# Kernel tuning notes

Measured on AMD Instinct MI355X. Metric: run time of the kernel, lower is better.

The kernel has to match this reference:

```python
import jax, jax.numpy as jnp
import numpy as np

B, S, D = 2, 2048, 2048
NH, NKV = 32, 8
HD = D // NH          # 64
NREP = NH // NKV      # 4


def _rope(x, cos, sin):
    # x: [B, S, H, HD]; cos/sin: [S, HD//2]
    x2 = x.reshape(*x.shape[:-1], HD // 2, 2)
    x0, x1 = x2[..., 0], x2[..., 1]
    c = cos[None, :, None, :]
    s = sin[None, :, None, :]
    r0 = x0 * c - x1 * s
    r1 = x0 * s + x1 * c
    return jnp.stack([r0, r1], axis=-1).reshape(x.shape)


def setup_inputs() -> dict:
    key = jax.random.key(0)
    ks = jax.random.split(key, 5)
    x = jax.random.normal(ks[0], (B, S, D), dtype=jnp.float32)
    wq = jax.random.normal(ks[1], (D, NH * HD), dtype=jnp.float32) * (D ** -0.5)
    wk = jax.random.normal(ks[2], (D, NKV * HD), dtype=jnp.float32) * (D ** -0.5)
    wv = jax.random.normal(ks[3], (D, NKV * HD), dtype=jnp.float32) * (D ** -0.5)
    wo = jax.random.normal(ks[4], (NH * HD, D), dtype=jnp.float32) * (D ** -0.5)
    # standard RoPE frequencies: theta = 10000^(-2i/HD)
    inv_freq = 1.0 / (10000.0 ** (np.arange(0, HD, 2, dtype=np.float32) / HD))
    angles = np.arange(S, dtype=np.float32)[:, None] * inv_freq[None, :]  # [S, HD/2]
    freqs_cos = jnp.asarray(np.cos(angles))
    freqs_sin = jnp.asarray(np.sin(angles))
    return {"x": x, "freqs_cos": freqs_cos, "freqs_sin": freqs_sin,
            "wq": wq, "wk": wk, "wv": wv, "wo": wo}


def reference(x, freqs_cos, freqs_sin, wq, wk, wv, wo):
    b, s, _ = x.shape
    xq = (x @ wq).reshape(b, s, NH, HD)
    xk = (x @ wk).reshape(b, s, NKV, HD)
    xv = (x @ wv).reshape(b, s, NKV, HD)
    xq = _rope(xq, freqs_cos, freqs_sin)
    xk = _rope(xk, freqs_cos, freqs_sin)
    # GQA repeat_kv: expand kv heads to NH
    keys = jnp.repeat(xk, NREP, axis=2)    # [B, S, NH, HD]
    values = jnp.repeat(xv, NREP, axis=2)
    scores = jnp.einsum('bqhd,bkhd->bhqk', xq, keys) / jnp.sqrt(jnp.float32(HD))
    causal = jnp.tril(jnp.ones((s, s), dtype=bool))
    scores = jnp.where(causal[None, None], scores, -jnp.inf)
    attn = jax.nn.softmax(scores.astype(jnp.float32), axis=-1).astype(xq.dtype)
    out = jnp.einsum('bhqk,bkhd->bqhd', attn, values).reshape(b, s, NH * HD)
    return out @ wo
```

## Files before the change

### kernel.cpp

```cpp
#include <hip/hip_runtime.h>
#include <hip/hip_bf16.h>

#define S_LEN 2048
#define DMODEL 2048
#define N_H 32
#define N_KV 8
#define H_D 64
#define ROWS 4096
#define QKV_LD 3072

typedef __bf16 bf16x8 __attribute__((ext_vector_type(8)));
typedef float f32x4 __attribute__((ext_vector_type(4)));

static __device__ __forceinline__ unsigned short f2bf(float f) {
  unsigned int u = __float_as_uint(f);
  u += 0x7FFFu + ((u >> 16) & 1u);
  return (unsigned short)(u >> 16);
}
static __device__ __forceinline__ float bf2f(unsigned short s) {
  return __uint_as_float((unsigned int)s << 16);
}

static __device__ __forceinline__ void async16(const void* g, void* l) {
  __builtin_amdgcn_global_load_lds(
      (const __attribute__((address_space(1))) unsigned int*)g,
      (__attribute__((address_space(3))) unsigned int*)l, 16, 0, 0);
}

#define VMB(N)                                                    \
  do {                                                            \
    asm volatile("s_waitcnt vmcnt(" #N ")" ::: "memory");         \
    __builtin_amdgcn_s_barrier();                                 \
    asm volatile("" ::: "memory");                                \
  } while (0)

__global__ __launch_bounds__(256) void cvt_bf16_k(
    const float* __restrict__ in, unsigned short* __restrict__ out) {
  const size_t i = ((size_t)blockIdx.x * 256 + threadIdx.x) * 8;
  const float4 a = *(const float4*)&in[i];
  const float4 b = *(const float4*)&in[i + 4];
  union { unsigned short u[8]; uint4 v; } p;
  p.u[0] = f2bf(a.x); p.u[1] = f2bf(a.y); p.u[2] = f2bf(a.z); p.u[3] = f2bf(a.w);
  p.u[4] = f2bf(b.x); p.u[5] = f2bf(b.y); p.u[6] = f2bf(b.z); p.u[7] = f2bf(b.w);
  *(uint4*)&out[i] = p.v;
}

__global__ __launch_bounds__(256) void prep_all_k(
    const float* __restrict__ x, const float* __restrict__ wq,
    const float* __restrict__ wk, const float* __restrict__ wv,
    const float* __restrict__ wo, unsigned short* __restrict__ xb,
    unsigned short* __restrict__ wqkvT, unsigned short* __restrict__ woT) {
  const int z = blockIdx.z;
  if (z == 4) {
    const size_t i =
        (((size_t)blockIdx.y * 64 + blockIdx.x) * 256 + threadIdx.x) * 8;
    const float4 a = *(const float4*)&x[i];
    const float4 b = *(const float4*)&x[i + 4];
    union { unsigned short u[8]; uint4 v; } p;
    p.u[0] = f2bf(a.x); p.u[1] = f2bf(a.y); p.u[2] = f2bf(a.z); p.u[3] = f2bf(a.w);
    p.u[4] = f2bf(b.x); p.u[5] = f2bf(b.y); p.u[6] = f2bf(b.z); p.u[7] = f2bf(b.w);
    *(uint4*)&xb[i] = p.v;
    return;
  }
  const float* in;
  unsigned short* out;
  int C;
  if (z == 0)      { in = wq; out = wqkvT;                  C = 2048; }
  else if (z == 1) { in = wk; out = wqkvT + 2048ull * 2048; C = 512;  }
  else if (z == 2) { in = wv; out = wqkvT + 2560ull * 2048; C = 512;  }
  else             { in = wo; out = woT;                    C = 2048; }
  if (blockIdx.x * 32 >= C) return;

  __shared__ unsigned short tile[32][33];
  const int tx = threadIdx.x & 31;
  const int ty = threadIdx.x >> 5;
  const int r0 = blockIdx.y * 32;
  const int c0 = blockIdx.x * 32;
#pragma unroll
  for (int i = 0; i < 32; i += 8)
    tile[ty + i][tx] = f2bf(in[(size_t)(r0 + ty + i) * C + c0 + tx]);
  __syncthreads();
#pragma unroll
  for (int i = 0; i < 32; i += 8)
    out[(size_t)(c0 + ty + i) * 2048 + r0 + tx] = tile[tx][ty + i];
}

#define SCALE_LOG2E 0.18033688011112042f

__global__ __launch_bounds__(256) void rope_vt_k(
    unsigned short* __restrict__ qkv, unsigned short* __restrict__ vT,
    const float* __restrict__ fc, const float* __restrict__ fs) {
  const int blk = blockIdx.x;
  if (blk < 20480) {
    const int PQ = ROWS * N_H * (H_D / 2);
    const int PK = ROWS * N_KV * (H_D / 2);
    const int idx = blk * 256 + threadIdx.x;
    if (idx >= PQ + PK) return;
    unsigned short* base;
    float c, sn;
    bool isq;
    if (idx < PQ) {
      const int i = idx & 31;
      const int h = (idx >> 5) & 31;
      const int row = idx >> 10;
      const int s = row & (S_LEN - 1);
      c = fc[s * 32 + i];
      sn = fs[s * 32 + i];
      base = qkv + (size_t)row * QKV_LD + h * H_D + 2 * i;
      isq = true;
    } else {
      const int p = idx - PQ;
      const int i = p & 31;
      const int h = (p >> 5) & 7;
      const int row = p >> 8;
      const int s = row & (S_LEN - 1);
      c = fc[s * 32 + i];
      sn = fs[s * 32 + i];
      base = qkv + (size_t)row * QKV_LD + 2048 + h * H_D + 2 * i;
      isq = false;
    }
    const float x0 = bf2f(base[0]);
    const float x1 = bf2f(base[1]);
    const float sc = isq ? SCALE_LOG2E : 1.0f;
    base[0] = f2bf((x0 * c - x1 * sn) * sc);
    base[1] = f2bf((x0 * sn + x1 * c) * sc);
  } else {
    __shared__ unsigned short tile[32][33];
    const int t = blk - 20480;
    const int bx = t & 15;
    const int by = t >> 4;
    const unsigned short* in = qkv + 2560;
    const int tx = threadIdx.x & 31;
    const int ty = threadIdx.x >> 5;
    const int r0 = by * 32;
    const int c0 = bx * 32;
#pragma unroll
    for (int i = 0; i < 32; i += 8)
      tile[ty + i][tx] = in[(size_t)(r0 + ty + i) * QKV_LD + c0 + tx];
    __syncthreads();
#pragma unroll
    for (int i = 0; i < 32; i += 8)
      vT[(size_t)(c0 + ty + i) * ROWS + r0 + tx] = tile[tx][ty + i];
  }
}

template <int STORE_BF16>
__global__ __launch_bounds__(512, 2) void gemm8w_bt_k(
    const unsigned short* __restrict__ A, const unsigned short* __restrict__ BT,
    void* __restrict__ Cp, int M, int N, int K, int lda) {
  __shared__ __align__(16) unsigned short As[2][2][128 * 64];
  __shared__ __align__(16) unsigned short Bs[2][192 * 64];
  const int tid = threadIdx.x;
  const int wave = tid >> 6;
  const int lane = tid & 63;
  const int quad = lane >> 4;
  const int l16 = lane & 15;
  const int nwg = gridDim.x * gridDim.y;
  const int flat = blockIdx.y * gridDim.x + blockIdx.x;
  const int swz = (flat & 7) * (nwg >> 3) + (flat >> 3);
  const int m0 = (swz % gridDim.x) * 256;
  const int n0 = (swz / gridDim.x) * 192;
  const int ah = wave & 1;
  const int ag = wave >> 1;
  const int wn = (wave >> 1) * 48;
  const int rx = (l16 & 7) << 3;
  const int scol = ((lane & 7) * 8) ^ ((lane >> 3) << 3);
  const int srA = 8 * ag + (lane >> 3);
  const int srB = 8 * wave + (lane >> 3);
  const size_t abase = (size_t)(m0 + ah * 128) * lda;
  const size_t bbase = (size_t)n0 * K;
  f32x4 acc[8][3] = {};

#define STG_B(j, buf, kt)                                             \
  async16(&BT[bbase + (size_t)(64 * (j) + srB) * K + (kt) + scol],    \
          &Bs[buf][(64 * (j) + 8 * wave) * 64])
#define STG_A(j, buf, kt)                                             \
  async16(&A[abase + (size_t)(32 * (j) + srA) * lda + (kt) + scol],   \
          &As[buf][ah][(32 * (j) + 8 * ag) * 64])

  STG_B(0, 0, 0); STG_B(1, 0, 0); STG_B(2, 0, 0);
  STG_A(0, 0, 0); STG_A(1, 0, 0); STG_A(2, 0, 0); STG_A(3, 0, 0);

  const int NT = K >> 6;
  for (int t = 0; t < NT; ++t) {
    const int cur = t & 1, nxt = cur ^ 1;
    const int ktn = (t + 1 < NT) ? ((t + 1) << 6) : 0;
    const unsigned short* Ac = &As[cur][ah][0];
    const unsigned short* Bc = &Bs[cur][0];
    bf16x8 bf[3][2];

    VMB(3);
    {
      bf16x8 af[2][2];
#pragma unroll
      for (int n = 0; n < 3; n++)
#pragma unroll
        for (int kk = 0; kk < 2; kk++)
          bf[n][kk] = *(const bf16x8*)&Bc[(wn + n * 16 + l16) * 64 +
                                          ((kk * 32 + quad * 8) ^ rx)];
#pragma unroll
      for (int i = 0; i < 2; i++)
#pragma unroll
        for (int kk = 0; kk < 2; kk++)
          af[i][kk] = *(const bf16x8*)&Ac[((0 + i) * 16 + l16) * 64 +
                                          ((kk * 32 + quad * 8) ^ rx)];
      STG_B(0, nxt, ktn); STG_B(1, nxt, ktn);
      __builtin_amdgcn_s_setprio(1);
#pragma unroll
      for (int i = 0; i < 2; i++)
#pragma unroll
        for (int n = 0; n < 3; n++)
#pragma unroll
          for (int kk = 0; kk < 2; kk++)
            acc[0 + i][n] = __builtin_amdgcn_mfma_f32_16x16x32_bf16(
                af[i][kk], bf[n][kk], acc[0 + i][n], 0, 0, 0);
      __builtin_amdgcn_s_setprio(0);
    }

    VMB(4);
    {
      bf16x8 af[2][2];
#pragma unroll
      for (int i = 0; i < 2; i++)
#pragma unroll
        for (int kk = 0; kk < 2; kk++)
          af[i][kk] = *(const bf16x8*)&Ac[((2 + i) * 16 + l16) * 64 +
                                          ((kk * 32 + quad * 8) ^ rx)];
      STG_B(2, nxt, ktn); STG_A(0, nxt, ktn);
      __builtin_amdgcn_s_setprio(1);
#pragma unroll
      for (int i = 0; i < 2; i++)
#pragma unroll
        for (int n = 0; n < 3; n++)
#pragma unroll
          for (int kk = 0; kk < 2; kk++)
            acc[2 + i][n] = __builtin_amdgcn_mfma_f32_16x16x32_bf16(
                af[i][kk], bf[n][kk], acc[2 + i][n], 0, 0, 0);
      __builtin_amdgcn_s_setprio(0);
    }

    VMB(5);
    {
      bf16x8 af[2][2];
#pragma unroll
      for (int i = 0; i < 2; i++)
#pragma unroll
        for (int kk = 0; kk < 2; kk++)
          af[i][kk] = *(const bf16x8*)&Ac[((4 + i) * 16 + l16) * 64 +
                                          ((kk * 32 + quad * 8) ^ rx)];
      STG_A(1, nxt, ktn); STG_A(2, nxt, ktn);
      __builtin_amdgcn_s_setprio(1);
#pragma unroll
      for (int i = 0; i < 2; i++)
#pragma unroll
        for (int n = 0; n < 3; n++)
#pragma unroll
          for (int kk = 0; kk < 2; kk++)
            acc[4 + i][n] = __builtin_amdgcn_mfma_f32_16x16x32_bf16(
                af[i][kk], bf[n][kk], acc[4 + i][n], 0, 0, 0);
      __builtin_amdgcn_s_setprio(0);
    }

    VMB(6);
    {
      bf16x8 af[2][2];
#pragma unroll
      for (int i = 0; i < 2; i++)
#pragma unroll
        for (int kk = 0; kk < 2; kk++)
          af[i][kk] = *(const bf16x8*)&Ac[((6 + i) * 16 + l16) * 64 +
                                          ((kk * 32 + quad * 8) ^ rx)];
      STG_A(3, nxt, ktn);
      __builtin_amdgcn_s_setprio(1);
#pragma unroll
      for (int i = 0; i < 2; i++)
#pragma unroll
        for (int n = 0; n < 3; n++)
#pragma unroll
          for (int kk = 0; kk < 2; kk++)
            acc[6 + i][n] = __builtin_amdgcn_mfma_f32_16x16x32_bf16(
                af[i][kk], bf[n][kk], acc[6 + i][n], 0, 0, 0);
      __builtin_amdgcn_s_setprio(0);
    }
  }
#undef STG_A
#undef STG_B

#pragma unroll
  for (int f = 0; f < 8; f++) {
#pragma unroll
    for (int e = 0; e < 4; e++) {
      const int mrow = m0 + ah * 128 + f * 16 + quad * 4 + e;
#pragma unroll
      for (int n = 0; n < 3; n++) {
        const int ncol = n0 + wn + n * 16 + l16;
        const float val = acc[f][n][e];
        if (STORE_BF16) {
          ((unsigned short*)Cp)[(size_t)mrow * N + ncol] = f2bf(val);
        } else {
          ((float*)Cp)[(size_t)mrow * N + ncol] = val;
        }
      }
    }
  }
}

template <int STORE_BF16>
__global__ __launch_bounds__(512, 2) void gemm8n_bt_k(
    const unsigned short* __restrict__ A, const unsigned short* __restrict__ BT,
    void* __restrict__ Cp, int M, int N, int K, int lda) {
  __shared__ __align__(16) unsigned short As[2][2][128 * 64];
  __shared__ __align__(16) unsigned short Bs[2][128 * 64];
  const int tid = threadIdx.x;
  const int wave = tid >> 6;
  const int lane = tid & 63;
  const int quad = lane >> 4;
  const int l16 = lane & 15;
  const int nwg = gridDim.x * gridDim.y;
  const int flat = blockIdx.y * gridDim.x + blockIdx.x;
  const int swz = (flat & 7) * (nwg >> 3) + (flat >> 3);
  const int m0 = (swz % gridDim.x) * 256;
  const int n0 = (swz / gridDim.x) * 128;
  const int ah = wave & 1;
  const int ag = wave >> 1;
  const int wn = (wave >> 1) * 32;
  const int rx = (l16 & 7) << 3;
  const int scol = ((lane & 7) * 8) ^ ((lane >> 3) << 3);
  const int srA = 8 * ag + (lane >> 3);
  const int srB = 8 * wave + (lane >> 3);
  const size_t abase = (size_t)(m0 + ah * 128) * lda;
  const size_t bbase = (size_t)n0 * K;
  f32x4 acc[8][2] = {};

#define STG_B(j, buf, kt)                                             \
  async16(&BT[bbase + (size_t)(64 * (j) + srB) * K + (kt) + scol],    \
          &Bs[buf][(64 * (j) + 8 * wave) * 64])
#define STG_A(j, buf, kt)                                             \
  async16(&A[abase + (size_t)(32 * (j) + srA) * lda + (kt) + scol],   \
          &As[buf][ah][(32 * (j) + 8 * ag) * 64])

  STG_B(0, 0, 0); STG_B(1, 0, 0);
  STG_A(0, 0, 0); STG_A(1, 0, 0); STG_A(2, 0, 0); STG_A(3, 0, 0);

  const int NT = K >> 6;
  for (int t = 0; t < NT; ++t) {
    const int cur = t & 1, nxt = cur ^ 1;
    const int ktn = (t + 1 < NT) ? ((t + 1) << 6) : 0;
    const unsigned short* Ac = &As[cur][ah][0];
    const unsigned short* Bc = &Bs[cur][0];
    bf16x8 bf[2][2];

    VMB(3);
    {
      bf16x8 af[2][2];
#pragma unroll
      for (int n = 0; n < 2; n++)
#pragma unroll
        for (int kk = 0; kk < 2; kk++)
          bf[n][kk] = *(const bf16x8*)&Bc[(wn + n * 16 + l16) * 64 +
                                          ((kk * 32 + quad * 8) ^ rx)];
#pragma unroll
      for (int i = 0; i < 2; i++)
#pragma unroll
        for (int kk = 0; kk < 2; kk++)
          af[i][kk] = *(const bf16x8*)&Ac[((0 + i) * 16 + l16) * 64 +
                                          ((kk * 32 + quad * 8) ^ rx)];
      STG_B(0, nxt, ktn); STG_B(1, nxt, ktn);
      __builtin_amdgcn_s_setprio(1);
#pragma unroll
      for (int i = 0; i < 2; i++)
#pragma unroll
        for (int n = 0; n < 2; n++)
#pragma unroll
          for (int kk = 0; kk < 2; kk++)
            acc[0 + i][n] = __builtin_amdgcn_mfma_f32_16x16x32_bf16(
                af[i][kk], bf[n][kk], acc[0 + i][n], 0, 0, 0);
      __builtin_amdgcn_s_setprio(0);
    }

    VMB(4);
    {
      bf16x8 af[2][2];
#pragma unroll
      for (int i = 0; i < 2; i++)
#pragma unroll
        for (int kk = 0; kk < 2; kk++)
          af[i][kk] = *(const bf16x8*)&Ac[((2 + i) * 16 + l16) * 64 +
                                          ((kk * 32 + quad * 8) ^ rx)];
      STG_A(0, nxt, ktn); STG_A(1, nxt, ktn);
      __builtin_amdgcn_s_setprio(1);
#pragma unroll
      for (int i = 0; i < 2; i++)
#pragma unroll
        for (int n = 0; n < 2; n++)
#pragma unroll
          for (int kk = 0; kk < 2; kk++)
            acc[2 + i][n] = __builtin_amdgcn_mfma_f32_16x16x32_bf16(
                af[i][kk], bf[n][kk], acc[2 + i][n], 0, 0, 0);
      __builtin_amdgcn_s_setprio(0);
    }

    VMB(5);
    {
      bf16x8 af[2][2];
#pragma unroll
      for (int i = 0; i < 2; i++)
#pragma unroll
        for (int kk = 0; kk < 2; kk++)
          af[i][kk] = *(const bf16x8*)&Ac[((4 + i) * 16 + l16) * 64 +
                                          ((kk * 32 + quad * 8) ^ rx)];
      STG_A(2, nxt, ktn); STG_A(3, nxt, ktn);
      __builtin_amdgcn_s_setprio(1);
#pragma unroll
      for (int i = 0; i < 2; i++)
#pragma unroll
        for (int n = 0; n < 2; n++)
#pragma unroll
          for (int kk = 0; kk < 2; kk++)
            acc[4 + i][n] = __builtin_amdgcn_mfma_f32_16x16x32_bf16(
                af[i][kk], bf[n][kk], acc[4 + i][n], 0, 0, 0);
      __builtin_amdgcn_s_setprio(0);
    }

    VMB(6);
    {
      bf16x8 af[2][2];
#pragma unroll
      for (int i = 0; i < 2; i++)
#pragma unroll
        for (int kk = 0; kk < 2; kk++)
          af[i][kk] = *(const bf16x8*)&Ac[((6 + i) * 16 + l16) * 64 +
                                          ((kk * 32 + quad * 8) ^ rx)];
      __builtin_amdgcn_s_setprio(1);
#pragma unroll
      for (int i = 0; i < 2; i++)
#pragma unroll
        for (int n = 0; n < 2; n++)
#pragma unroll
          for (int kk = 0; kk < 2; kk++)
            acc[6 + i][n] = __builtin_amdgcn_mfma_f32_16x16x32_bf16(
                af[i][kk], bf[n][kk], acc[6 + i][n], 0, 0, 0);
      __builtin_amdgcn_s_setprio(0);
    }
  }
#undef STG_A
#undef STG_B

#pragma unroll
  for (int f = 0; f < 8; f++) {
#pragma unroll
    for (int e = 0; e < 4; e++) {
      const int mrow = m0 + ah * 128 + f * 16 + quad * 4 + e;
#pragma unroll
      for (int n = 0; n < 2; n++) {
        const int ncol = n0 + wn + n * 16 + l16;
        const float val = acc[f][n][e];
        if (STORE_BF16) {
          ((unsigned short*)Cp)[(size_t)mrow * N + ncol] = f2bf(val);
        } else {
          ((float*)Cp)[(size_t)mrow * N + ncol] = val;
        }
      }
    }
  }
}

template <int AF32, int STORE_BF16>
__global__ __launch_bounds__(256) void gemm_k(
    const void* __restrict__ Ap, const float* __restrict__ B,
    void* __restrict__ Cp, int M, int N, int K) {
  constexpr int LDP = 40;
  __shared__ __align__(16) unsigned short As[128 * LDP];
  __shared__ __align__(16) unsigned short Bs[128 * LDP];
  const int tid = threadIdx.x;
  const int wave = tid >> 6;
  const int lane = tid & 63;
  const int quad = lane >> 4;
  const int l16 = lane & 15;
  const int m0 = blockIdx.x * 128;
  const int n0 = blockIdx.y * 128;
  const int wm = (wave >> 1) * 64;
  const int wn = (wave & 1) * 64;
  f32x4 acc[4][4] = {};

  for (int kt = 0; kt < K; kt += 32) {
    __syncthreads();
    if (AF32) {
      const float* A = (const float*)Ap;
      for (int c = tid; c < 1024; c += 256) {
        const int r = c >> 3;
        const int cc = (c & 7) << 2;
        const float4 w = *(const float4*)&A[(size_t)(m0 + r) * K + kt + cc];
        union { unsigned short u[4]; uint2 v; } p;
        p.u[0] = f2bf(w.x); p.u[1] = f2bf(w.y);
        p.u[2] = f2bf(w.z); p.u[3] = f2bf(w.w);
        *(uint2*)&As[r * LDP + cc] = p.v;
      }
    } else {
      const unsigned short* A = (const unsigned short*)Ap;
      for (int c = tid; c < 512; c += 256) {
        const int r = c >> 2;
        const int cc = (c & 3) << 3;
        *(uint4*)&As[r * LDP + cc] =
            *(const uint4*)&A[(size_t)(m0 + r) * K + kt + cc];
      }
    }
    for (int c = tid; c < 1024; c += 256) {
      const int kr = c >> 5;
      const int nc = (c & 31) << 2;
      const float4 w = *(const float4*)&B[(size_t)(kt + kr) * N + n0 + nc];
      Bs[(nc + 0) * LDP + kr] = f2bf(w.x);
      Bs[(nc + 1) * LDP + kr] = f2bf(w.y);
      Bs[(nc + 2) * LDP + kr] = f2bf(w.z);
      Bs[(nc + 3) * LDP + kr] = f2bf(w.w);
    }
    __syncthreads();
    bf16x8 af[4], bfr[4];
#pragma unroll
    for (int i = 0; i < 4; i++)
      af[i] = *(const bf16x8*)&As[(wm + i * 16 + l16) * LDP + quad * 8];
#pragma unroll
    for (int j = 0; j < 4; j++)
      bfr[j] = *(const bf16x8*)&Bs[(wn + j * 16 + l16) * LDP + quad * 8];
#pragma unroll
    for (int i = 0; i < 4; i++)
#pragma unroll
      for (int j = 0; j < 4; j++)
        acc[i][j] =
            __builtin_amdgcn_mfma_f32_16x16x32_bf16(af[i], bfr[j], acc[i][j], 0, 0, 0);
  }
#pragma unroll
  for (int i = 0; i < 4; i++) {
#pragma unroll
    for (int e = 0; e < 4; e++) {
      const int mrow = m0 + wm + i * 16 + quad * 4 + e;
#pragma unroll
      for (int j = 0; j < 4; j++) {
        const int ncol = n0 + wn + j * 16 + l16;
        const float val = acc[i][j][e];
        if (STORE_BF16) {
          ((unsigned short*)Cp)[(size_t)mrow * N + ncol] = f2bf(val);
        } else {
          ((float*)Cp)[(size_t)mrow * N + ncol] = val;
        }
      }
    }
  }
}

__global__ __launch_bounds__(256) void rope_k(
    unsigned short* __restrict__ q, unsigned short* __restrict__ kk,
    const float* __restrict__ fc, const float* __restrict__ fs,
    int qstride, int kstride) {
  const int PQ = ROWS * N_H * (H_D / 2);
  const int PK = ROWS * N_KV * (H_D / 2);
  const int idx = blockIdx.x * 256 + threadIdx.x;
  if (idx >= PQ + PK) return;
  unsigned short* base;
  float c, sn;
  if (idx < PQ) {
    const int i = idx & 31;
    const int h = (idx >> 5) & 31;
    const int row = idx >> 10;
    const int s = row & (S_LEN - 1);
    c = fc[s * 32 + i];
    sn = fs[s * 32 + i];
    base = q + (size_t)row * qstride + h * H_D + 2 * i;
  } else {
    const int p = idx - PQ;
    const int i = p & 31;
    const int h = (p >> 5) & 7;
    const int row = p >> 8;
    const int s = row & (S_LEN - 1);
    c = fc[s * 32 + i];
    sn = fs[s * 32 + i];
    base = kk + (size_t)row * kstride + h * H_D + 2 * i;
  }
  const float x0 = bf2f(base[0]);
  const float x1 = bf2f(base[1]);
  base[0] = f2bf(x0 * c - x1 * sn);
  base[1] = f2bf(x0 * sn + x1 * c);
}

__global__ __launch_bounds__(512, 4) void attn_mfma13_k(
    const unsigned short* __restrict__ qkv, const unsigned short* __restrict__ vT,
    unsigned short* __restrict__ ao) {
  const int pair = blockIdx.x, h = blockIdx.y, b = blockIdx.z;
  const int hk = h >> 2;
  const int tid = threadIdx.x;
  const int wave = tid >> 6;
  const int l16 = tid & 15;
  const int quad = (tid & 63) >> 4;
  const int rr = tid >> 3;
  const int dc = (tid & 7) * 8;
  const int rx = (l16 & 7) << 3;
  const int sx = (rr & 7) << 3;

  __shared__ __align__(16) unsigned short Ks[2][64 * 64];
  __shared__ __align__(16) unsigned short Vt[2][64 * 64];
  __shared__ __align__(16) unsigned short Ps[8][16 * 64];

  bf16x8 ones;
#pragma unroll
  for (int j = 0; j < 8; j++) ones[j] = (__bf16)1.0f;

  const size_t kbase =
      (size_t)(b * S_LEN) * QKV_LD + 2048 + hk * H_D + dc;
  const size_t vbase = (size_t)(hk * H_D + rr) * ROWS + b * S_LEN + dc;

  for (int sel = 0; sel < 2; ++sel) {
    const int qb = sel ? (15 - pair) : pair;
    const int row0 = qb * 128;
    const int ktiles = 2 * qb + 2;

    bf16x8 af[2];
    {
      const size_t qrow = (size_t)(b * S_LEN + row0 + wave * 16 + l16);
#pragma unroll
      for (int c = 0; c < 2; c++)
        af[c] =
            *(const bf16x8*)&qkv[qrow * QKV_LD + h * H_D + c * 32 + quad * 8];
    }

    f32x4 o_acc[4] = {};
    f32x4 l_acc = {};

    uint4 rk, rv;
    {
      rk = *(const uint4*)&qkv[kbase + (size_t)rr * QKV_LD];
      rv = *(const uint4*)&vT[vbase];
    }
    __syncthreads();
    *(uint4*)&Ks[0][rr * 64 + (dc ^ sx)] = rk;
    *(uint4*)&Vt[0][rr * 64 + (dc ^ sx)] = rv;

    int cur = 0;
    for (int kt = 0; kt < ktiles; ++kt) {
      if (kt + 1 < ktiles) {
        rk = *(const uint4*)&qkv[kbase + (size_t)((kt + 1) * 64 + rr) * QKV_LD];
        rv = *(const uint4*)&vT[vbase + (size_t)(kt + 1) * 64];
      }
      __syncthreads();

      f32x4 sacc[4];
#pragma unroll
      for (int n = 0; n < 4; n++) {
        f32x4 z = {};
#pragma unroll
        for (int c = 0; c < 2; c++) {
          const bf16x8 bk = *(const bf16x8*)&Ks[cur][(n * 16 + l16) * 64 +
                                                     ((c * 32 + quad * 8) ^ rx)];
          z = __builtin_amdgcn_mfma_f32_16x16x32_bf16(bk, af[c], z, 0, 0, 0);
        }
        sacc[n] = z;
      }

      const bool maybe_mask = (kt >= 2 * qb);
      {
        const int prow = l16 * 64;
        if (maybe_mask) {
          const int krel0 = (kt - 2 * qb) * 64;
          const int qn = wave * 16 + l16;
#pragma unroll
          for (int n = 0; n < 4; n++) {
            const int kb0 = krel0 + n * 16 + quad * 4;
            float pe[4];
#pragma unroll
            for (int e = 0; e < 4; e++) {
              float v = exp2f(sacc[n][e]);
              if (kb0 + e > qn) v = 0.f;
              pe[e] = v;
            }
            uint2 u;
            u.x = __builtin_amdgcn_perm(__float_as_uint(pe[1]),
                                        __float_as_uint(pe[0]), 0x07060302u);
            u.y = __builtin_amdgcn_perm(__float_as_uint(pe[3]),
                                        __float_as_uint(pe[2]), 0x07060302u);
            *(uint2*)&Ps[wave][prow + ((n * 16 + quad * 4) ^ rx)] = u;
          }
        } else {
#pragma unroll
          for (int n = 0; n < 4; n++) {
            float pe[4];
#pragma unroll
            for (int e = 0; e < 4; e++) pe[e] = exp2f(sacc[n][e]);
            uint2 u;
            u.x = __builtin_amdgcn_perm(__float_as_uint(pe[1]),
                                        __float_as_uint(pe[0]), 0x07060302u);
            u.y = __builtin_amdgcn_perm(__float_as_uint(pe[3]),
                                        __float_as_uint(pe[2]), 0x07060302u);
            *(uint2*)&Ps[wave][prow + ((n * 16 + quad * 4) ^ rx)] = u;
          }
        }
      }

      bf16x8 pf[2];
#pragma unroll
      for (int c = 0; c < 2; c++)
        pf[c] = *(const bf16x8*)&Ps[wave][l16 * 64 +
                                          ((c * 32 + quad * 8) ^ rx)];
#pragma unroll
      for (int c = 0; c < 2; c++)
        l_acc = __builtin_amdgcn_mfma_f32_16x16x32_bf16(pf[c], ones, l_acc,
                                                        0, 0, 0);
#pragma unroll
      for (int n = 0; n < 4; n++)
#pragma unroll
        for (int c = 0; c < 2; c++) {
          const bf16x8 bv = *(const bf16x8*)&Vt[cur][(n * 16 + l16) * 64 +
                                                     ((c * 32 + quad * 8) ^ rx)];
          o_acc[n] = __builtin_amdgcn_mfma_f32_16x16x32_bf16(pf[c], bv,
                                                             o_acc[n], 0, 0, 0);
        }

      if (kt + 1 < ktiles) {
        const int nxt = cur ^ 1;
        *(uint4*)&Ks[nxt][rr * 64 + (dc ^ sx)] = rk;
        *(uint4*)&Vt[nxt][rr * 64 + (dc ^ sx)] = rv;
      }
      cur ^= 1;
    }

#pragma unroll
    for (int e = 0; e < 4; e++) {
      const float inv = 1.f / l_acc[e];
      const size_t row =
          (size_t)(b * S_LEN + row0 + wave * 16 + quad * 4 + e);
#pragma unroll
      for (int n = 0; n < 4; n++)
        ao[row * QKV_LD + h * H_D + n * 16 + l16] = f2bf(o_acc[n][e] * inv);
    }
  }
}

#define LK 72

__global__ __launch_bounds__(256) void attn_mfma_k(
    const unsigned short* __restrict__ q, const unsigned short* __restrict__ k,
    const unsigned short* __restrict__ v, unsigned short* __restrict__ ao) {
  const int qt = blockIdx.x, h = blockIdx.y, b = blockIdx.z;
  const int hk = h >> 2;
  const int tid = threadIdx.x;
  const int wave = tid >> 6;
  const int l16 = tid & 15;
  const int quad = (tid & 63) >> 4;

  __shared__ __align__(16) unsigned short Ks[64 * LK];
  __shared__ __align__(16) unsigned short Vt[64 * LK];
  __shared__ __align__(16) unsigned short Ps[64 * LK];

  bf16x8 af[2];
  {
    const size_t qrow = (size_t)(b * S_LEN + qt * 64 + wave * 16 + l16);
#pragma unroll
    for (int c = 0; c < 2; c++)
      af[c] = *(const bf16x8*)&q[qrow * DMODEL + h * H_D + c * 32 + quad * 8];
  }

  f32x4 o_acc[4] = {};
  float m_i[4], l_i[4];
#pragma unroll
  for (int e = 0; e < 4; e++) { m_i[e] = -INFINITY; l_i[e] = 0.f; }

  for (int kt = 0; kt <= qt; ++kt) {
    const int kb = kt * 64;
    __syncthreads();
    {
      const int kr = tid >> 2;
      const int dc = (tid & 3) * 16;
      const size_t gro = (size_t)(b * S_LEN + kb + kr) * (N_KV * H_D) + hk * H_D + dc;
      *(uint4*)&Ks[kr * LK + dc] = *(const uint4*)&k[gro];
      *(uint4*)&Ks[kr * LK + dc + 8] = *(const uint4*)&k[gro + 8];
      union { unsigned short u[8]; uint4 v; } w0, w1;
      w0.v = *(const uint4*)&v[gro];
      w1.v = *(const uint4*)&v[gro + 8];
#pragma unroll
      for (int j = 0; j < 8; j++) Vt[(dc + j) * LK + kr] = w0.u[j];
#pragma unroll
      for (int j = 0; j < 8; j++) Vt[(dc + 8 + j) * LK + kr] = w1.u[j];
    }
    __syncthreads();

    f32x4 sacc[4];
#pragma unroll
    for (int n = 0; n < 4; n++) {
      f32x4 z = {};
#pragma unroll
      for (int c = 0; c < 2; c++) {
        const bf16x8 bk = *(const bf16x8*)&Ks[(n * 16 + l16) * LK + c * 32 + quad * 8];
        z = __builtin_amdgcn_mfma_f32_16x16x32_bf16(af[c], bk, z, 0, 0, 0);
      }
      sacc[n] = z;
    }

    float p[4][4], mnew[4];
#pragma unroll
    for (int e = 0; e < 4; e++) mnew[e] = m_i[e];
#pragma unroll
    for (int n = 0; n < 4; n++)
#pragma unroll
      for (int e = 0; e < 4; e++) {
        float s = sacc[n][e] * 0.125f;
        if (kt == qt && (n * 16 + l16) > (wave * 16 + quad * 4 + e))
          s = -INFINITY;
        p[n][e] = s;
        mnew[e] = fmaxf(mnew[e], s);
      }
#pragma unroll
    for (int e = 0; e < 4; e++) {
      mnew[e] = fmaxf(mnew[e], __shfl_xor(mnew[e], 1));
      mnew[e] = fmaxf(mnew[e], __shfl_xor(mnew[e], 2));
      mnew[e] = fmaxf(mnew[e], __shfl_xor(mnew[e], 4));
      mnew[e] = fmaxf(mnew[e], __shfl_xor(mnew[e], 8));
      const float alpha = __expf(m_i[e] - mnew[e]);
      m_i[e] = mnew[e];
      l_i[e] *= alpha;
#pragma unroll
      for (int n = 0; n < 4; n++) o_acc[n][e] *= alpha;
    }
#pragma unroll
    for (int n = 0; n < 4; n++)
#pragma unroll
      for (int e = 0; e < 4; e++) {
        const float pe = __expf(p[n][e] - m_i[e]);
        p[n][e] = pe;
        l_i[e] += pe;
      }

#pragma unroll
    for (int n = 0; n < 4; n++)
#pragma unroll
      for (int e = 0; e < 4; e++)
        Ps[(wave * 16 + quad * 4 + e) * LK + n * 16 + l16] = f2bf(p[n][e]);
    __syncthreads();

    bf16x8 pf[2];
#pragma unroll
    for (int c = 0; c < 2; c++)
      pf[c] = *(const bf16x8*)&Ps[(wave * 16 + l16) * LK + c * 32 + quad * 8];
#pragma unroll
    for (int n = 0; n < 4; n++)
#pragma unroll
      for (int c = 0; c < 2; c++) {
        const bf16x8 bv = *(const bf16x8*)&Vt[(n * 16 + l16) * LK + c * 32 + quad * 8];
        o_acc[n] = __builtin_amdgcn_mfma_f32_16x16x32_bf16(pf[c], bv, o_acc[n], 0, 0, 0);
      }
  }

#pragma unroll
  for (int e = 0; e < 4; e++) {
    l_i[e] += __shfl_xor(l_i[e], 1);
    l_i[e] += __shfl_xor(l_i[e], 2);
    l_i[e] += __shfl_xor(l_i[e], 4);
    l_i[e] += __shfl_xor(l_i[e], 8);
    const float inv = 1.f / l_i[e];
    const size_t row = (size_t)(b * S_LEN + qt * 64 + wave * 16 + quad * 4 + e);
#pragma unroll
    for (int n = 0; n < 4; n++)
      ao[row * DMODEL + h * H_D + n * 16 + l16] = f2bf(o_acc[n][e] * inv);
  }
}

extern "C" void kernel_launch(void* const* d_in, const int* in_sizes, int n_in,
                              void* d_out, int out_size, void* d_ws, size_t ws_size,
                              hipStream_t stream) {
  const float* x = (const float*)d_in[0];
  const float* fc = (const float*)d_in[1];
  const float* fs = (const float*)d_in[2];
  const float* wq = (const float*)d_in[3];
  const float* wk = (const float*)d_in[4];
  const float* wv = (const float*)d_in[5];
  const float* wo = (const float*)d_in[6];

  char* ws = (char*)d_ws;
  const dim3 b256(256);

  if (ws_size >= (64ull << 20)) {
    unsigned short* qkv = (unsigned short*)(ws);
    unsigned short* xb = (unsigned short*)(ws + (24ull << 20));
    unsigned short* wqkvT = (unsigned short*)(ws + (40ull << 20));
    unsigned short* woT = (unsigned short*)(ws + (52ull << 20));
    unsigned short* vT = (unsigned short*)(ws + (60ull << 20));

    prep_all_k<<<dim3(64, 64, 5), b256, 0, stream>>>(x, wq, wk, wv, wo, xb,
                                                     wqkvT, woT);

    gemm8w_bt_k<1><<<dim3(16, 16), dim3(512), 0, stream>>>(xb, wqkvT, qkv, 4096,
                                                           3072, 2048, 2048);

    rope_vt_k<<<dim3(20480 + 2048), b256, 0, stream>>>(qkv, vT, fc, fs);

    attn_mfma13_k<<<dim3(8, N_H, 2), dim3(512), 0, stream>>>(qkv, vT, qkv);

    gemm8n_bt_k<0><<<dim3(16, 16), dim3(512), 0, stream>>>(qkv, woT, d_out,
                                                           4096, 2048, 2048,
                                                           QKV_LD);
  } else {
    unsigned short* q = (unsigned short*)(ws);
    unsigned short* k = (unsigned short*)(ws + (16ull << 20));
    unsigned short* v = (unsigned short*)(ws + (20ull << 20));
    unsigned short* xb = (unsigned short*)(ws + (24ull << 20));
    const bool have_xb = ws_size >= (40ull << 20);

    if (have_xb) {
      cvt_bf16_k<<<dim3(ROWS * DMODEL / (256 * 8)), b256, 0, stream>>>(x, xb);
      gemm_k<0, 1><<<dim3(32, 16), b256, 0, stream>>>(xb, wq, q, 4096, 2048, 2048);
      gemm_k<0, 1><<<dim3(32, 4), b256, 0, stream>>>(xb, wk, k, 4096, 512, 2048);
      gemm_k<0, 1><<<dim3(32, 4), b256, 0, stream>>>(xb, wv, v, 4096, 512, 2048);
    } else {
      gemm_k<1, 1><<<dim3(32, 16), b256, 0, stream>>>(x, wq, q, 4096, 2048, 2048);
      gemm_k<1, 1><<<dim3(32, 4), b256, 0, stream>>>(x, wk, k, 4096, 512, 2048);
      gemm_k<1, 1><<<dim3(32, 4), b256, 0, stream>>>(x, wv, v, 4096, 512, 2048);
    }

    rope_k<<<dim3(20480), b256, 0, stream>>>(q, k, fc, fs, N_H * H_D, N_KV * H_D);
    attn_mfma_k<<<dim3(S_LEN / 64, N_H, 2), b256, 0, stream>>>(q, k, v, q);
    gemm_k<0, 0><<<dim3(32, 16), b256, 0, stream>>>(q, wo, d_out, 4096, 2048, 2048);
  }
}
```

Before: 275.9 us.

## Software-pipeline attention PV with next tile's QK^T using triple-buffered V

Restructures the attention inner loop so the P·V product (and row-sum) for the previous key tile runs after the QK^T MFMAs of the current tile. The exp/softmax work of one tile can then overlap matrix-core work from another. V tiles move to a three-slot rotating LDS buffer so the previous tile's V stays valid while the next one is stored. Launch bounds relax from 4 to 2 blocks per SM, which allows more registers but may cut occupancy. LDS use also grows.

```diff
diff --git a/kernel.cpp b/kernel.cpp
--- a/kernel.cpp
+++ b/kernel.cpp
@@ -582,7 +582,7 @@
   base[1] = f2bf(x0 * sn + x1 * c);
 }
 
-__global__ __launch_bounds__(512, 4) void attn_mfma13_k(
+__global__ __launch_bounds__(512, 2) void attn_mfma14_k(
     const unsigned short* __restrict__ qkv, const unsigned short* __restrict__ vT,
     unsigned short* __restrict__ ao) {
   const int pair = blockIdx.x, h = blockIdx.y, b = blockIdx.z;
@@ -597,7 +597,7 @@
   const int sx = (rr & 7) << 3;
 
   __shared__ __align__(16) unsigned short Ks[2][64 * 64];
-  __shared__ __align__(16) unsigned short Vt[2][64 * 64];
+  __shared__ __align__(16) unsigned short Vt[3][64 * 64];
   __shared__ __align__(16) unsigned short Ps[8][16 * 64];
 
   bf16x8 ones;
@@ -624,6 +624,7 @@
 
     f32x4 o_acc[4] = {};
     f32x4 l_acc = {};
+    bf16x8 pf[2];
 
     uint4 rk, rv;
     {
@@ -634,7 +635,7 @@
     *(uint4*)&Ks[0][rr * 64 + (dc ^ sx)] = rk;
     *(uint4*)&Vt[0][rr * 64 + (dc ^ sx)] = rv;
 
-    int cur = 0;
+    int vprev = 2, vnxt = 1;
     for (int kt = 0; kt < ktiles; ++kt) {
       if (kt + 1 < ktiles) {
         rk = *(const uint4*)&qkv[kbase + (size_t)((kt + 1) * 64 + rr) * QKV_LD];
@@ -643,16 +644,36 @@
       __syncthreads();
 
       f32x4 sacc[4];
-#pragma unroll
-      for (int n = 0; n < 4; n++) {
-        f32x4 z = {};
-#pragma unroll
-        for (int c = 0; c < 2; c++) {
-          const bf16x8 bk = *(const bf16x8*)&Ks[cur][(n * 16 + l16) * 64 +
-                                                     ((c * 32 + quad * 8) ^ rx)];
-          z = __builtin_amdgcn_mfma_f32_16x16x32_bf16(bk, af[c], z, 0, 0, 0);
+      {
+        const unsigned short* Kc = &Ks[kt & 1][0];
+#pragma unroll
+        for (int n = 0; n < 4; n++) {
+          f32x4 z = {};
+#pragma unroll
+          for (int c = 0; c < 2; c++) {
+            const bf16x8 bk = *(const bf16x8*)&Kc[(n * 16 + l16) * 64 +
+                                                  ((c * 32 + quad * 8) ^ rx)];
+            z = __builtin_amdgcn_mfma_f32_16x16x32_bf16(bk, af[c], z, 0, 0, 0);
+          }
+          sacc[n] = z;
         }
-        sacc[n] = z;
+      }
+
+      if (kt > 0) {
+        const unsigned short* Vc = &Vt[vprev][0];
+#pragma unroll
+        for (int c = 0; c < 2; c++)
+          l_acc = __builtin_amdgcn_mfma_f32_16x16x32_bf16(pf[c], ones, l_acc,
+                                                          0, 0, 0);
+#pragma unroll
+        for (int n = 0; n < 4; n++)
+#pragma unroll
+          for (int c = 0; c < 2; c++) {
+            const bf16x8 bv = *(const bf16x8*)&Vc[(n * 16 + l16) * 64 +
+                                                  ((c * 32 + quad * 8) ^ rx)];
+            o_acc[n] = __builtin_amdgcn_mfma_f32_16x16x32_bf16(pf[c], bv,
+                                                               o_acc[n], 0, 0, 0);
+          }
       }
 
       const bool maybe_mask = (kt >= 2 * qb);
@@ -693,12 +714,21 @@
           }
         }
       }
-
-      bf16x8 pf[2];
 #pragma unroll
       for (int c = 0; c < 2; c++)
         pf[c] = *(const bf16x8*)&Ps[wave][l16 * 64 +
                                           ((c * 32 + quad * 8) ^ rx)];
+
+      if (kt + 1 < ktiles) {
+        *(uint4*)&Ks[(kt + 1) & 1][rr * 64 + (dc ^ sx)] = rk;
+        *(uint4*)&Vt[vnxt][rr * 64 + (dc ^ sx)] = rv;
+      }
+      vprev = (vprev == 2) ? 0 : vprev + 1;
+      vnxt = (vnxt == 2) ? 0 : vnxt + 1;
+    }
+
+    {
+      const unsigned short* Vc = &Vt[vprev][0];
 #pragma unroll
       for (int c = 0; c < 2; c++)
         l_acc = __builtin_amdgcn_mfma_f32_16x16x32_bf16(pf[c], ones, l_acc,
@@ -707,18 +737,11 @@
       for (int n = 0; n < 4; n++)
 #pragma unroll
         for (int c = 0; c < 2; c++) {
-          const bf16x8 bv = *(const bf16x8*)&Vt[cur][(n * 16 + l16) * 64 +
-                                                     ((c * 32 + quad * 8) ^ rx)];
+          const bf16x8 bv = *(const bf16x8*)&Vc[(n * 16 + l16) * 64 +
+                                                ((c * 32 + quad * 8) ^ rx)];
           o_acc[n] = __builtin_amdgcn_mfma_f32_16x16x32_bf16(pf[c], bv,
                                                              o_acc[n], 0, 0, 0);
         }
-
-      if (kt + 1 < ktiles) {
-        const int nxt = cur ^ 1;
-        *(uint4*)&Ks[nxt][rr * 64 + (dc ^ sx)] = rk;
-        *(uint4*)&Vt[nxt][rr * 64 + (dc ^ sx)] = rv;
-      }
-      cur ^= 1;
     }
 
 #pragma unroll
@@ -890,7 +913,7 @@
 
     rope_vt_k<<<dim3(20480 + 2048), b256, 0, stream>>>(qkv, vT, fc, fs);
 
-    attn_mfma13_k<<<dim3(8, N_H, 2), dim3(512), 0, stream>>>(qkv, vT, qkv);
+    attn_mfma14_k<<<dim3(8, N_H, 2), dim3(512), 0, stream>>>(qkv, vT, qkv);
 
     gemm8n_bt_k<0><<<dim3(16, 16), dim3(512), 0, stream>>>(qkv, woT, d_out,
                                                            4096, 2048, 2048,
```

Result: no change. 278.6 us (+1.0%).
